# Performance work log

Hardware: AMD Instinct MI355X
Metric: run time of the kernel (lower is better)

Reference implementation:

```python
import jax, jax.numpy as jnp
import numpy as np

B, S, D, H = 2, 2048, 1024, 16
DH = D // H  # dim_per_head = 64


def setup_inputs() -> dict:
    key = jax.random.key(0)
    ks = jax.random.split(key, 12)
    scale = 1.0 / np.sqrt(D)
    inp = {
        "key": jax.random.normal(ks[0], (B, S, D), jnp.float32),
        "value": jax.random.normal(ks[1], (B, S, D), jnp.float32),
        "query": jax.random.normal(ks[2], (B, S, D), jnp.float32),
        "mask": jax.random.randint(ks[3], (B, S, S), 0, 2) == 1,
        "Wq": jax.random.normal(ks[4], (D, D), jnp.float32) * scale,
        "bq": jnp.zeros((D,), jnp.float32),
        "Wk": jax.random.normal(ks[5], (D, D), jnp.float32) * scale,
        "bk": jnp.zeros((D,), jnp.float32),
        "Wv": jax.random.normal(ks[6], (D, D), jnp.float32) * scale,
        "bv": jnp.zeros((D,), jnp.float32),
        "Wo": jax.random.normal(ks[7], (D, D), jnp.float32) * scale,
        "bo": jnp.zeros((D,), jnp.float32),
    }
    return inp


def reference(key, value, query, mask, Wq, bq, Wk, bk, Wv, bv, Wo, bo):
    b, s, d = query.shape
    dh = d // H

    def split_heads(x):  # [b, s, d] -> [b, H, s, dh]
        return x.reshape(b, -1, H, dh).transpose(0, 2, 1, 3)

    q = split_heads(query @ Wq + bq) / jnp.sqrt(jnp.float32(dh))
    k = split_heads(key @ Wk + bk)
    v = split_heads(value @ Wv + bv)

    scores = jnp.einsum("bhqd,bhkd->bhqk", q, k)  # [b, H, s, s]
    scores = jnp.where(mask[:, None, :, :], jnp.float32(-1e18), scores)
    attn = jax.nn.softmax(scores, axis=-1)  # dropout is identity in eval
    ctx = jnp.einsum("bhqk,bhkd->bhqd", attn, v)
    ctx = ctx.transpose(0, 2, 1, 3).reshape(b, s, d)
    return ctx @ Wo + bo
```

## Files before the change

### kernel.cpp

```cpp
#include <hip/hip_runtime.h>
#include <hip/hip_bf16.h>

#define BATCH  2
#define SEQ    2048
#define DMODEL 1024
#define NHEAD  16
#define DHEAD  64
#define NTOK   (BATCH * SEQ)

using f32x4 = __attribute__((ext_vector_type(4))) float;
using s16x4 = __attribute__((ext_vector_type(4))) short;
using s16x8 = __attribute__((ext_vector_type(8))) short;

__device__ __forceinline__ short f2bf(float f) {
  __hip_bfloat16 h = __float2bfloat16(f);
  return *(short*)&h;
}

__device__ __forceinline__ void gload_lds16(const short* g, short* l) {
  __builtin_amdgcn_global_load_lds(
      (const __attribute__((address_space(1))) void*)g,
      (__attribute__((address_space(3))) void*)l, 16, 0, 0);
}

__global__ __launch_bounds__(256) void wtrans_kernel(
    const float* __restrict__ Wq, const float* __restrict__ Wk,
    const float* __restrict__ Wv, const float* __restrict__ Wo,
    short* __restrict__ Wt) {
  __shared__ short tile[64][72];
  const float* W = blockIdx.z == 0 ? Wq : blockIdx.z == 1 ? Wk
                 : blockIdx.z == 2 ? Wv : Wo;
  short* out = Wt + (size_t)blockIdx.z * DMODEL * DMODEL;
  int k0 = blockIdx.x * 64, n0 = blockIdx.y * 64;
  int t = threadIdx.x;
#pragma unroll
  for (int i = 0; i < 4; ++i) {
    int idx = t + i * 256;
    int row = idx >> 4, c4 = idx & 15;
    f32x4 v = *(const f32x4*)(W + (size_t)(k0 + row) * DMODEL + n0 + c4 * 4);
    s16x4 p;
    p[0] = f2bf(v[0]); p[1] = f2bf(v[1]); p[2] = f2bf(v[2]); p[3] = f2bf(v[3]);
    *(s16x4*)&tile[row][c4 * 4] = p;
  }
  __syncthreads();
#pragma unroll
  for (int i = 0; i < 2; ++i) {
    int idx = t + i * 256;
    int nrow = idx >> 3, c8 = idx & 7;
    s16x8 p;
#pragma unroll
    for (int j = 0; j < 8; ++j) p[j] = tile[c8 * 8 + j][nrow];
    *(s16x8*)(out + (size_t)(n0 + nrow) * DMODEL + k0 + c8 * 8) = p;
  }
}

__global__ __launch_bounds__(256) void xcast_kernel(
    const float* __restrict__ Xq, const float* __restrict__ Xk,
    const float* __restrict__ Xv, short* __restrict__ Xb) {
  int sel = blockIdx.y;
  const float* src = sel == 0 ? Xq : sel == 1 ? Xk : Xv;
  size_t off = ((size_t)blockIdx.x * 256 + threadIdx.x) * 8;
  f32x4 v0 = *(const f32x4*)(src + off);
  f32x4 v1 = *(const f32x4*)(src + off + 4);
  s16x8 p;
  p[0] = f2bf(v0[0]); p[1] = f2bf(v0[1]); p[2] = f2bf(v0[2]); p[3] = f2bf(v0[3]);
  p[4] = f2bf(v1[0]); p[5] = f2bf(v1[1]); p[6] = f2bf(v1[2]); p[7] = f2bf(v1[3]);
  *(s16x8*)(Xb + (size_t)sel * NTOK * DMODEL + off) = p;
}

__global__ __launch_bounds__(256) void mpack_kernel(
    const int* __restrict__ mask, unsigned long long* __restrict__ Mp) {
  const int total_words = BATCH * SEQ * (SEQ / 64);
  int lane = threadIdx.x & 63;
  int wv = blockIdx.x * 4 + (threadIdx.x >> 6);
  int nw = gridDim.x * 4;
  for (int w = wv; w < total_words; w += nw) {
    int mv = mask[(size_t)w * 64 + lane];
    unsigned long long bits = __ballot(mv != 0);
    if (lane == 0) Mp[w] = bits;
  }
}

__global__ __launch_bounds__(256) void proj_qkv_kernel(
    const short* __restrict__ Xb, const short* __restrict__ Wt,
    const float* __restrict__ bq, const float* __restrict__ bk,
    const float* __restrict__ bv, short* __restrict__ QKV) {
  __shared__ short As[2][128 * 32];
  __shared__ short Bs[2][128 * 32];
  int wg = blockIdx.x;
  int orig = (wg & 7) * 96 + (wg >> 3);
  int sel = orig >> 8;
  int rem = orig & 255;
  int mx = rem >> 3, ny = rem & 7;

  const short* X    = Xb + (size_t)sel * NTOK * DMODEL;
  const float* bias = sel == 0 ? bq : sel == 1 ? bk : bv;
  const short* Wsel = Wt + (size_t)sel * DMODEL * DMODEL;
  short* Obuf = QKV + (size_t)sel * ((size_t)BATCH * NHEAD * SEQ * DHEAD);
  const float scale = sel == 0 ? 0.18033688011111793f : 1.0f;

  int m0 = mx * 128, n0 = ny * 128;
  int t = threadIdx.x, wid = t >> 6, lane = t & 63;
  int lr = lane & 15, lg = lane >> 4;
  int wr = wid >> 1, wc = wid & 1;
  f32x4 acc[4][4] = {};

  const int gr0 = t >> 2, gc0 = (t & 3) << 3;
  const short* Ax0 = X + (size_t)(m0 + gr0) * DMODEL + gc0;
  const short* Ax1 = Ax0 + (size_t)64 * DMODEL;
  const short* Bw0 = Wsel + (size_t)(n0 + gr0) * DMODEL + gc0;
  const short* Bw1 = Bw0 + (size_t)64 * DMODEL;
  const int lofs0 = (t & ~63) << 3, lofs1 = lofs0 + 256 * 8;

#define STAGEQ(bufi, k0s) {                                                   \
    gload_lds16(Ax0 + (k0s), &As[bufi][0] + lofs0);                           \
    gload_lds16(Ax1 + (k0s), &As[bufi][0] + lofs1);                           \
    gload_lds16(Bw0 + (k0s), &Bs[bufi][0] + lofs0);                           \
    gload_lds16(Bw1 + (k0s), &Bs[bufi][0] + lofs1); }

  STAGEQ(0, 0);
  __syncthreads();

  int cur = 0;
  for (int kt = 0; kt < DMODEL / 32; ++kt) {
    if (kt + 1 < DMODEL / 32) STAGEQ(cur ^ 1, (kt + 1) * 32);
    s16x8 afr[4], bfr[4];
#pragma unroll
    for (int mi = 0; mi < 4; ++mi)
      afr[mi] = *(const s16x8*)(&As[cur][0] + (wr * 64 + mi * 16 + lr) * 32 + lg * 8);
#pragma unroll
    for (int ni = 0; ni < 4; ++ni)
      bfr[ni] = *(const s16x8*)(&Bs[cur][0] + (wc * 64 + ni * 16 + lr) * 32 + lg * 8);
    __builtin_amdgcn_s_setprio(1);
#pragma unroll
    for (int mi = 0; mi < 4; ++mi)
#pragma unroll
      for (int ni = 0; ni < 4; ++ni)
        acc[mi][ni] = __builtin_amdgcn_mfma_f32_16x16x32_bf16(
            afr[mi], bfr[ni], acc[mi][ni], 0, 0, 0);
    __builtin_amdgcn_s_setprio(0);
    __syncthreads();
    cur ^= 1;
  }
#undef STAGEQ

  if (sel == 2) {
    int bq_ = m0 >> 11;
    int s0 = (m0 & (SEQ - 1)) + wr * 64 + lg * 4;
#pragma unroll
    for (int mi = 0; mi < 4; ++mi)
#pragma unroll
      for (int ni = 0; ni < 4; ++ni) {
        int n = n0 + wc * 64 + ni * 16 + lr;
        float bv_ = bias[n];
        int h = n >> 6, d = n & 63;
        s16x4 pk;
#pragma unroll
        for (int r = 0; r < 4; ++r) pk[r] = f2bf(acc[mi][ni][r] + bv_);
        *(s16x4*)&Obuf[((size_t)(bq_ * NHEAD + h) * DHEAD + d) * SEQ
                       + s0 + mi * 16] = pk;
      }
  } else {
#pragma unroll
    for (int mi = 0; mi < 4; ++mi)
#pragma unroll
      for (int ni = 0; ni < 4; ++ni) {
        int n = n0 + wc * 64 + ni * 16 + lr;
        float bv_ = bias[n];
        int h = n >> 6, d = n & 63;
#pragma unroll
        for (int r = 0; r < 4; ++r) {
          int m = m0 + wr * 64 + mi * 16 + lg * 4 + r;
          int b = m >> 11, s = m & (SEQ - 1);
          float val = (acc[mi][ni][r] + bv_) * scale;
          Obuf[((size_t)(b * NHEAD + h) * SEQ + s) * DHEAD + d] = f2bf(val);
        }
      }
  }
}

__global__ __launch_bounds__(256) void attn_kernel(
    const short* __restrict__ Qb, const short* __restrict__ Kb,
    const short* __restrict__ VbT, const unsigned long long* __restrict__ Mp,
    short* __restrict__ Ctx) {
  __shared__ short Ks[2][64 * 64];
  __shared__ short Vt[2][64 * 64];
  __shared__ short Ps[4 * 16 * 64];
  int wg = blockIdx.x;
  int orig = (wg & 7) * 128 + (wg >> 3);
  int bh = orig >> 5, qt = orig & 31;
  int b = bh >> 4, h = bh & 15;
  int q0 = qt * 64;
  int t = threadIdx.x, wid = t >> 6, lane = t & 63;
  int lr = lane & 15, lg = lane >> 4;
  int lr7 = lr & 7;

  const short* Qrow = Qb + ((size_t)bh * SEQ + q0 + wid * 16 + lr) * DHEAD;
  s16x8 qf[2];
  qf[0] = *(const s16x8*)(Qrow + lg * 8);
  qf[1] = *(const s16x8*)(Qrow + 32 + lg * 8);

  const short* KbB = Kb + (size_t)bh * SEQ * DHEAD;
  const short* VtB = VbT + (size_t)bh * DHEAD * SEQ;

  const int srow = lane >> 3;
  const int schunk = ((lane & 7) ^ srow) * 8;

  float m_run = -1e30f, l_run = 0.f;
  f32x4 o_acc[4] = {};

  const unsigned long long* mrow =
      Mp + ((size_t)b * SEQ + q0 + wid * 16 + lr) * (SEQ / 64);

#define STAGE(bufi, k0s)                                                      \
  {                                                                           \
    _Pragma("unroll")                                                         \
    for (int i = 0; i < 2; ++i) {                                             \
      int rbase = wid * 16 + i * 8;                                           \
      gload_lds16(KbB + (size_t)((k0s) + rbase + srow) * DHEAD + schunk,      \
                  &Ks[bufi][rbase * 64]);                                     \
      gload_lds16(VtB + (size_t)(rbase + srow) * SEQ + (k0s) + schunk,        \
                  &Vt[bufi][rbase * 64]);                                     \
    }                                                                         \
  }

  unsigned long long mw_cur = mrow[0];
  STAGE(0, 0);
  asm volatile("s_waitcnt vmcnt(0)" ::: "memory");
  __syncthreads();

  int cur = 0;
  for (int kt = 0; kt < SEQ / 64; ++kt) {
    unsigned long long mw_next = 0;
    if (kt + 1 < SEQ / 64) {
      STAGE(cur ^ 1, (kt + 1) * 64);
      mw_next = mrow[kt + 1];
    }
    const short* KsC = Ks[cur];
    const short* VtC = Vt[cur];

    f32x4 sfr[4];
    __builtin_amdgcn_s_setprio(1);
#pragma unroll
    for (int nf = 0; nf < 4; ++nf) {
      int row = nf * 16 + lr;
      s16x8 kf0 = *(const s16x8*)&KsC[row * 64 + ((lg ^ lr7) << 3)];
      s16x8 kf1 = *(const s16x8*)&KsC[row * 64 + (((4 + lg) ^ lr7) << 3)];
      f32x4 c = {};
      c = __builtin_amdgcn_mfma_f32_16x16x32_bf16(kf0, qf[0], c, 0, 0, 0);
      c = __builtin_amdgcn_mfma_f32_16x16x32_bf16(kf1, qf[1], c, 0, 0, 0);
      sfr[nf] = c;
    }
    __builtin_amdgcn_s_setprio(0);

    unsigned w0 = (unsigned)(mw_cur >> (lg * 4));
    unsigned w1 = (unsigned)(mw_cur >> (lg * 4 + 32));
#pragma unroll
    for (int nf = 0; nf < 4; ++nf)
#pragma unroll
      for (int r = 0; r < 4; ++r) {
        unsigned bit = (nf < 2) ? (w0 >> (nf * 16 + r)) : (w1 >> ((nf - 2) * 16 + r));
        if (bit & 1u) sfr[nf][r] = -1e30f;
      }
    float tm = fmaxf(fmaxf(fmaxf(sfr[0][0], sfr[0][1]), fmaxf(sfr[0][2], sfr[0][3])),
                     fmaxf(fmaxf(sfr[1][0], sfr[1][1]), fmaxf(sfr[1][2], sfr[1][3])));
    float tm2 = fmaxf(fmaxf(fmaxf(sfr[2][0], sfr[2][1]), fmaxf(sfr[2][2], sfr[2][3])),
                      fmaxf(fmaxf(sfr[3][0], sfr[3][1]), fmaxf(sfr[3][2], sfr[3][3])));
    tm = fmaxf(tm, tm2);
    tm = fmaxf(tm, __shfl_xor(tm, 16, 64));
    tm = fmaxf(tm, __shfl_xor(tm, 32, 64));

    bool small = __all(tm <= m_run + 8.0f);
    if (!small) {
      float mnew = fmaxf(m_run, tm);
      float scl = __builtin_amdgcn_exp2f(m_run - mnew);
      m_run = mnew;
      l_run *= scl;
      float scl_o[4];
#pragma unroll
      for (int r = 0; r < 4; ++r) scl_o[r] = __shfl(scl, lg * 4 + r, 64);
#pragma unroll
      for (int nf = 0; nf < 4; ++nf)
#pragma unroll
        for (int r = 0; r < 4; ++r) o_acc[nf][r] *= scl_o[r];
    }
    float ps4[4];
#pragma unroll
    for (int nf = 0; nf < 4; ++nf) {
#pragma unroll
      for (int r = 0; r < 4; ++r)
        sfr[nf][r] = __builtin_amdgcn_exp2f(sfr[nf][r] - m_run);
      ps4[nf] = (sfr[nf][0] + sfr[nf][1]) + (sfr[nf][2] + sfr[nf][3]);
    }
    float ps = (ps4[0] + ps4[1]) + (ps4[2] + ps4[3]);
    ps += __shfl_xor(ps, 16, 64);
    ps += __shfl_xor(ps, 32, 64);
    l_run += ps;

    int psbase = wid * (16 * 64) + lr * 64;
#pragma unroll
    for (int nf = 0; nf < 4; ++nf) {
      s16x4 pk;
#pragma unroll
      for (int r = 0; r < 4; ++r) pk[r] = f2bf(sfr[nf][r]);
      *(s16x4*)&Ps[psbase + ((((2 * nf + (lg >> 1)) ^ lr7) << 3) | ((lg & 1) << 2))] = pk;
    }
    asm volatile("s_waitcnt lgkmcnt(0)" ::: "memory");
    __builtin_amdgcn_sched_barrier(0);

    __builtin_amdgcn_s_setprio(1);
#pragma unroll
    for (int ks = 0; ks < 2; ++ks) {
      s16x8 pf = *(const s16x8*)&Ps[psbase + (((ks * 4 + lg) ^ lr7) << 3)];
#pragma unroll
      for (int nf = 0; nf < 4; ++nf) {
        int d = nf * 16 + lr;
        s16x8 vf = *(const s16x8*)&VtC[d * 64 + (((ks * 4 + lg) ^ lr7) << 3)];
        o_acc[nf] = __builtin_amdgcn_mfma_f32_16x16x32_bf16(pf, vf, o_acc[nf], 0, 0, 0);
      }
    }
    __builtin_amdgcn_s_setprio(0);

    asm volatile("s_waitcnt vmcnt(0)" ::: "memory");
    __syncthreads();
    cur ^= 1;
    mw_cur = mw_next;
  }
#undef STAGE
  float l_o[4];
#pragma unroll
  for (int r = 0; r < 4; ++r) l_o[r] = __shfl(l_run, lg * 4 + r, 64);
#pragma unroll
  for (int nf = 0; nf < 4; ++nf)
#pragma unroll
    for (int r = 0; r < 4; ++r) {
      int srow_ = q0 + wid * 16 + lg * 4 + r;
      float val = o_acc[nf][r] / l_o[r];
      Ctx[((size_t)b * SEQ + srow_) * DMODEL + h * DHEAD + nf * 16 + lr] = f2bf(val);
    }
}

__global__ __launch_bounds__(256) void proj_out_kernel(
    const short* __restrict__ Ctx, const short* __restrict__ Wot,
    const float* __restrict__ bo, float* __restrict__ Out) {
  __shared__ short As[2][128 * 32];
  __shared__ short Bs[2][128 * 32];
  int wg = blockIdx.x;
  int orig = (wg & 7) * 32 + (wg >> 3);
  int mx = orig >> 3, ny = orig & 7;
  int m0 = mx * 128, n0 = ny * 128;
  int t = threadIdx.x, wid = t >> 6, lane = t & 63;
  int lr = lane & 15, lg = lane >> 4;
  int wr = wid >> 1, wc = wid & 1;
  f32x4 acc[4][4] = {};

  const int gr0 = t >> 2, gc0 = (t & 3) << 3;
  const short* Actx0 = Ctx + (size_t)(m0 + gr0) * DMODEL + gc0;
  const short* Actx1 = Actx0 + (size_t)64 * DMODEL;
  const short* Bwo0 = Wot + (size_t)(n0 + gr0) * DMODEL + gc0;
  const short* Bwo1 = Bwo0 + (size_t)64 * DMODEL;
  const int lofs0 = (t & ~63) << 3, lofs1 = lofs0 + 256 * 8;

#define STAGE_PO(bufi, k0s) {                                                 \
    gload_lds16(Actx0 + (k0s), &As[bufi][0] + lofs0);                         \
    gload_lds16(Actx1 + (k0s), &As[bufi][0] + lofs1);                         \
    gload_lds16(Bwo0 + (k0s), &Bs[bufi][0] + lofs0);                          \
    gload_lds16(Bwo1 + (k0s), &Bs[bufi][0] + lofs1); }

  STAGE_PO(0, 0);
  __syncthreads();

  int cur = 0;
  for (int kt = 0; kt < DMODEL / 32; ++kt) {
    if (kt + 1 < DMODEL / 32) STAGE_PO(cur ^ 1, (kt + 1) * 32);
    s16x8 afr[4], bfr[4];
#pragma unroll
    for (int mi = 0; mi < 4; ++mi)
      afr[mi] = *(const s16x8*)(&As[cur][0] + (wr * 64 + mi * 16 + lr) * 32 + lg * 8);
#pragma unroll
    for (int ni = 0; ni < 4; ++ni)
      bfr[ni] = *(const s16x8*)(&Bs[cur][0] + (wc * 64 + ni * 16 + lr) * 32 + lg * 8);
    __builtin_amdgcn_s_setprio(1);
#pragma unroll
    for (int mi = 0; mi < 4; ++mi)
#pragma unroll
      for (int ni = 0; ni < 4; ++ni)
        acc[mi][ni] = __builtin_amdgcn_mfma_f32_16x16x32_bf16(
            afr[mi], bfr[ni], acc[mi][ni], 0, 0, 0);
    __builtin_amdgcn_s_setprio(0);
    __syncthreads();
    cur ^= 1;
  }
#undef STAGE_PO

#pragma unroll
  for (int mi = 0; mi < 4; ++mi)
#pragma unroll
    for (int ni = 0; ni < 4; ++ni) {
      int n = n0 + wc * 64 + ni * 16 + lr;
      float bv_ = bo[n];
#pragma unroll
      for (int r = 0; r < 4; ++r) {
        int m = m0 + wr * 64 + mi * 16 + lg * 4 + r;
        Out[(size_t)m * DMODEL + n] = acc[mi][ni][r] + bv_;
      }
    }
}

extern "C" void kernel_launch(void* const* d_in, const int* in_sizes, int n_in,
                              void* d_out, int out_size, void* d_ws, size_t ws_size,
                              hipStream_t stream) {
  const float* key_in   = (const float*)d_in[0];
  const float* value_in = (const float*)d_in[1];
  const float* query_in = (const float*)d_in[2];
  const int*   mask     = (const int*)d_in[3];
  const float* Wq = (const float*)d_in[4];
  const float* bq = (const float*)d_in[5];
  const float* Wk = (const float*)d_in[6];
  const float* bk = (const float*)d_in[7];
  const float* Wv = (const float*)d_in[8];
  const float* bv = (const float*)d_in[9];
  const float* Wo = (const float*)d_in[10];
  const float* bo = (const float*)d_in[11];
  float* out = (float*)d_out;

  short* ws = (short*)d_ws;
  const size_t WSZ   = (size_t)DMODEL * DMODEL;
  const size_t QKVSZ = (size_t)BATCH * NHEAD * SEQ * DHEAD;
  const size_t XSZ   = (size_t)NTOK * DMODEL;
  short* Wt  = ws;
  short* QKV = ws + 4 * WSZ;
  short* Qb  = QKV;
  short* Kb  = QKV + QKVSZ;
  short* VbT = QKV + 2 * QKVSZ;
  short* Xb  = ws + 4 * WSZ + 3 * QKVSZ;
  short* Ctx = Xb;
  unsigned long long* Mp = (unsigned long long*)ws;

  wtrans_kernel<<<dim3(16, 16, 4), 256, 0, stream>>>(Wq, Wk, Wv, Wo, Wt);
  xcast_kernel<<<dim3(2048, 3), 256, 0, stream>>>(query_in, key_in, value_in, Xb);
  proj_qkv_kernel<<<dim3(768), 256, 0, stream>>>(Xb, Wt, bq, bk, bv, QKV);
  mpack_kernel<<<dim3(1024), 256, 0, stream>>>(mask, Mp);
  attn_kernel<<<dim3(1024), 256, 0, stream>>>(Qb, Kb, VbT, Mp, Ctx);
  proj_out_kernel<<<dim3(256), 256, 0, stream>>>(Ctx, Wt + 3 * WSZ, bo, out);
}
```

Baseline: 189.0 us.

## Use 32x32x16 MFMA in attention with register-resident P and 128-row query tiles

Rewrites the attention kernel so each wave handles 32 query rows with 32x32x16 bf16 MFMAs instead of 16 rows with 16x16x32. The S^T accumulator layout lets P be packed straight from registers into the PV MFMA operand, which removes the LDS round trip and its waitcnt for P. Each workgroup now covers 128 query rows, so the grid is halved and each K/V tile staged in LDS is reused by twice as many queries. The costs are fewer workgroups (512) and larger 16-wide accumulators that raise register pressure, plus more per-element shuffles when rescaling.

New measurement: 183.9 us. -2.7%, faster.

```diff
diff --git a/kernel.cpp b/kernel.cpp
--- a/kernel.cpp
+++ b/kernel.cpp
@@ -8,9 +8,10 @@
 #define DHEAD  64
 #define NTOK   (BATCH * SEQ)
 
-using f32x4 = __attribute__((ext_vector_type(4))) float;
-using s16x4 = __attribute__((ext_vector_type(4))) short;
-using s16x8 = __attribute__((ext_vector_type(8))) short;
+using f32x4  = __attribute__((ext_vector_type(4))) float;
+using f32x16 = __attribute__((ext_vector_type(16))) float;
+using s16x4  = __attribute__((ext_vector_type(4))) short;
+using s16x8  = __attribute__((ext_vector_type(8))) short;
 
 __device__ __forceinline__ short f2bf(float f) {
   __hip_bfloat16 h = __float2bfloat16(f);
@@ -185,20 +186,19 @@
     short* __restrict__ Ctx) {
   __shared__ short Ks[2][64 * 64];
   __shared__ short Vt[2][64 * 64];
-  __shared__ short Ps[4 * 16 * 64];
   int wg = blockIdx.x;
-  int orig = (wg & 7) * 128 + (wg >> 3);
-  int bh = orig >> 5, qt = orig & 31;
+  int orig = (wg & 7) * 64 + (wg >> 3);
+  int bh = orig >> 4, qt = orig & 15;
   int b = bh >> 4, h = bh & 15;
-  int q0 = qt * 64;
+  int q0 = qt * 128;
   int t = threadIdx.x, wid = t >> 6, lane = t & 63;
-  int lr = lane & 15, lg = lane >> 4;
-  int lr7 = lr & 7;
-
-  const short* Qrow = Qb + ((size_t)bh * SEQ + q0 + wid * 16 + lr) * DHEAD;
-  s16x8 qf[2];
-  qf[0] = *(const s16x8*)(Qrow + lg * 8);
-  qf[1] = *(const s16x8*)(Qrow + 32 + lg * 8);
+  int ql = lane & 31, hi = lane >> 5;
+  int qrow = q0 + wid * 32 + ql;
+
+  const short* Qp = Qb + ((size_t)bh * SEQ + qrow) * DHEAD + hi * 8;
+  s16x8 qf[4];
+#pragma unroll
+  for (int ds = 0; ds < 4; ++ds) qf[ds] = *(const s16x8*)(Qp + ds * 16);
 
   const short* KbB = Kb + (size_t)bh * SEQ * DHEAD;
   const short* VtB = VbT + (size_t)bh * DHEAD * SEQ;
@@ -206,11 +206,21 @@
   const int srow = lane >> 3;
   const int schunk = ((lane & 7) ^ srow) * 8;
 
+  int offK[4];
+#pragma unroll
+  for (int j = 0; j < 4; ++j)
+    offK[j] = ql * 64 + (((j * 2 + hi) ^ (ql & 7)) << 3);
+  int offVa[4], offVb[4];
+#pragma unroll
+  for (int m = 0; m < 4; ++m) {
+    offVa[m] = ql * 64 + (((m * 2)     ^ (ql & 7)) << 3) + 4 * hi;
+    offVb[m] = ql * 64 + (((m * 2 + 1) ^ (ql & 7)) << 3) + 4 * hi;
+  }
+
   float m_run = -1e30f, l_run = 0.f;
-  f32x4 o_acc[4] = {};
-
-  const unsigned long long* mrow =
-      Mp + ((size_t)b * SEQ + q0 + wid * 16 + lr) * (SEQ / 64);
+  f32x16 oacc0 = {}, oacc1 = {};
+
+  const unsigned long long* mrow = Mp + ((size_t)b * SEQ + qrow) * (SEQ / 64);
 
 #define STAGE(bufi, k0s)                                                      \
   {                                                                           \
@@ -239,35 +249,31 @@
     const short* KsC = Ks[cur];
     const short* VtC = Vt[cur];
 
-    f32x4 sfr[4];
+    f32x16 sf0 = {}, sf1 = {};
     __builtin_amdgcn_s_setprio(1);
 #pragma unroll
-    for (int nf = 0; nf < 4; ++nf) {
-      int row = nf * 16 + lr;
-      s16x8 kf0 = *(const s16x8*)&KsC[row * 64 + ((lg ^ lr7) << 3)];
-      s16x8 kf1 = *(const s16x8*)&KsC[row * 64 + (((4 + lg) ^ lr7) << 3)];
-      f32x4 c = {};
-      c = __builtin_amdgcn_mfma_f32_16x16x32_bf16(kf0, qf[0], c, 0, 0, 0);
-      c = __builtin_amdgcn_mfma_f32_16x16x32_bf16(kf1, qf[1], c, 0, 0, 0);
-      sfr[nf] = c;
+    for (int ds = 0; ds < 4; ++ds) {
+      s16x8 k0 = *(const s16x8*)&KsC[offK[ds]];
+      s16x8 k1 = *(const s16x8*)&KsC[offK[ds] + 2048];
+      sf0 = __builtin_amdgcn_mfma_f32_32x32x16_bf16(k0, qf[ds], sf0, 0, 0, 0);
+      sf1 = __builtin_amdgcn_mfma_f32_32x32x16_bf16(k1, qf[ds], sf1, 0, 0, 0);
     }
     __builtin_amdgcn_s_setprio(0);
 
-    unsigned w0 = (unsigned)(mw_cur >> (lg * 4));
-    unsigned w1 = (unsigned)(mw_cur >> (lg * 4 + 32));
-#pragma unroll
-    for (int nf = 0; nf < 4; ++nf)
-#pragma unroll
-      for (int r = 0; r < 4; ++r) {
-        unsigned bit = (nf < 2) ? (w0 >> (nf * 16 + r)) : (w1 >> ((nf - 2) * 16 + r));
-        if (bit & 1u) sfr[nf][r] = -1e30f;
-      }
-    float tm = fmaxf(fmaxf(fmaxf(sfr[0][0], sfr[0][1]), fmaxf(sfr[0][2], sfr[0][3])),
-                     fmaxf(fmaxf(sfr[1][0], sfr[1][1]), fmaxf(sfr[1][2], sfr[1][3])));
-    float tm2 = fmaxf(fmaxf(fmaxf(sfr[2][0], sfr[2][1]), fmaxf(sfr[2][2], sfr[2][3])),
-                      fmaxf(fmaxf(sfr[3][0], sfr[3][1]), fmaxf(sfr[3][2], sfr[3][3])));
-    tm = fmaxf(tm, tm2);
-    tm = fmaxf(tm, __shfl_xor(tm, 16, 64));
+    unsigned h0 = ((unsigned)mw_cur) >> (hi << 2);
+    unsigned h1 = ((unsigned)(mw_cur >> 32)) >> (hi << 2);
+#pragma unroll
+    for (int r = 0; r < 16; ++r) {
+      const int c = (r & 3) + 8 * (r >> 2);
+      if ((h0 >> c) & 1u) sf0[r] = -1e30f;
+      if ((h1 >> c) & 1u) sf1[r] = -1e30f;
+    }
+
+    float tm = sf0[0];
+#pragma unroll
+    for (int r = 1; r < 16; ++r) tm = fmaxf(tm, sf0[r]);
+#pragma unroll
+    for (int r = 0; r < 16; ++r) tm = fmaxf(tm, sf1[r]);
     tm = fmaxf(tm, __shfl_xor(tm, 32, 64));
 
     bool small = __all(tm <= m_run + 8.0f);
@@ -276,48 +282,38 @@
       float scl = __builtin_amdgcn_exp2f(m_run - mnew);
       m_run = mnew;
       l_run *= scl;
-      float scl_o[4];
-#pragma unroll
-      for (int r = 0; r < 4; ++r) scl_o[r] = __shfl(scl, lg * 4 + r, 64);
-#pragma unroll
-      for (int nf = 0; nf < 4; ++nf)
-#pragma unroll
-        for (int r = 0; r < 4; ++r) o_acc[nf][r] *= scl_o[r];
-    }
-    float ps4[4];
-#pragma unroll
-    for (int nf = 0; nf < 4; ++nf) {
-#pragma unroll
-      for (int r = 0; r < 4; ++r)
-        sfr[nf][r] = __builtin_amdgcn_exp2f(sfr[nf][r] - m_run);
-      ps4[nf] = (sfr[nf][0] + sfr[nf][1]) + (sfr[nf][2] + sfr[nf][3]);
-    }
-    float ps = (ps4[0] + ps4[1]) + (ps4[2] + ps4[3]);
-    ps += __shfl_xor(ps, 16, 64);
-    ps += __shfl_xor(ps, 32, 64);
-    l_run += ps;
-
-    int psbase = wid * (16 * 64) + lr * 64;
-#pragma unroll
-    for (int nf = 0; nf < 4; ++nf) {
-      s16x4 pk;
-#pragma unroll
-      for (int r = 0; r < 4; ++r) pk[r] = f2bf(sfr[nf][r]);
-      *(s16x4*)&Ps[psbase + ((((2 * nf + (lg >> 1)) ^ lr7) << 3) | ((lg & 1) << 2))] = pk;
-    }
-    asm volatile("s_waitcnt lgkmcnt(0)" ::: "memory");
-    __builtin_amdgcn_sched_barrier(0);
+#pragma unroll
+      for (int r = 0; r < 16; ++r) {
+        float s_ = __shfl(scl, (r & 3) + 8 * (r >> 2) + 4 * hi, 64);
+        oacc0[r] *= s_;
+        oacc1[r] *= s_;
+      }
+    }
+
+    float ss = 0.f;
+#pragma unroll
+    for (int r = 0; r < 16; ++r) {
+      sf0[r] = __builtin_amdgcn_exp2f(sf0[r] - m_run);
+      sf1[r] = __builtin_amdgcn_exp2f(sf1[r] - m_run);
+      ss += sf0[r] + sf1[r];
+    }
+    l_run += ss + __shfl_xor(ss, 32, 64);
 
     __builtin_amdgcn_s_setprio(1);
 #pragma unroll
-    for (int ks = 0; ks < 2; ++ks) {
-      s16x8 pf = *(const s16x8*)&Ps[psbase + (((ks * 4 + lg) ^ lr7) << 3)];
-#pragma unroll
-      for (int nf = 0; nf < 4; ++nf) {
-        int d = nf * 16 + lr;
-        s16x8 vf = *(const s16x8*)&VtC[d * 64 + (((ks * 4 + lg) ^ lr7) << 3)];
-        o_acc[nf] = __builtin_amdgcn_mfma_f32_16x16x32_bf16(pf, vf, o_acc[nf], 0, 0, 0);
-      }
+    for (int m = 0; m < 4; ++m) {
+      const int base = (m & 1) * 8;
+      s16x8 pa;
+#pragma unroll
+      for (int e = 0; e < 8; ++e)
+        pa[e] = f2bf(m < 2 ? sf0[base + e] : sf1[base + e]);
+      union { s16x4 q[2]; s16x8 v; } v0, v1;
+      v0.q[0] = *(const s16x4*)&VtC[offVa[m]];
+      v0.q[1] = *(const s16x4*)&VtC[offVb[m]];
+      v1.q[0] = *(const s16x4*)&VtC[offVa[m] + 2048];
+      v1.q[1] = *(const s16x4*)&VtC[offVb[m] + 2048];
+      oacc0 = __builtin_amdgcn_mfma_f32_32x32x16_bf16(pa, v0.v, oacc0, 0, 0, 0);
+      oacc1 = __builtin_amdgcn_mfma_f32_32x32x16_bf16(pa, v1.v, oacc1, 0, 0, 0);
     }
     __builtin_amdgcn_s_setprio(0);
 
@@ -327,17 +323,16 @@
     mw_cur = mw_next;
   }
 #undef STAGE
-  float l_o[4];
-#pragma unroll
-  for (int r = 0; r < 4; ++r) l_o[r] = __shfl(l_run, lg * 4 + r, 64);
-#pragma unroll
-  for (int nf = 0; nf < 4; ++nf)
-#pragma unroll
-    for (int r = 0; r < 4; ++r) {
-      int srow_ = q0 + wid * 16 + lg * 4 + r;
-      float val = o_acc[nf][r] / l_o[r];
-      Ctx[((size_t)b * SEQ + srow_) * DMODEL + h * DHEAD + nf * 16 + lr] = f2bf(val);
-    }
+
+#pragma unroll
+  for (int r = 0; r < 16; ++r) {
+    int c = (r & 3) + 8 * (r >> 2) + 4 * hi;
+    float linv = 1.0f / __shfl(l_run, c, 64);
+    int q_ = q0 + wid * 32 + c;
+    size_t base = ((size_t)b * SEQ + q_) * DMODEL + h * DHEAD + ql;
+    Ctx[base] = f2bf(oacc0[r] * linv);
+    Ctx[base + 32] = f2bf(oacc1[r] * linv);
+  }
 }
 
 __global__ __launch_bounds__(256) void proj_out_kernel(
@@ -427,7 +422,6 @@
   short* ws = (short*)d_ws;
   const size_t WSZ   = (size_t)DMODEL * DMODEL;
   const size_t QKVSZ = (size_t)BATCH * NHEAD * SEQ * DHEAD;
-  const size_t XSZ   = (size_t)NTOK * DMODEL;
   short* Wt  = ws;
   short* QKV = ws + 4 * WSZ;
   short* Qb  = QKV;
@@ -441,6 +435,6 @@
   xcast_kernel<<<dim3(2048, 3), 256, 0, stream>>>(query_in, key_in, value_in, Xb);
   proj_qkv_kernel<<<dim3(768), 256, 0, stream>>>(Xb, Wt, bq, bk, bv, QKV);
   mpack_kernel<<<dim3(1024), 256, 0, stream>>>(mask, Mp);
-  attn_kernel<<<dim3(1024), 256, 0, stream>>>(Qb, Kb, VbT, Mp, Ctx);
+  attn_kernel<<<dim3(512), 256, 0, stream>>>(Qb, Kb, VbT, Mp, Ctx);
   proj_out_kernel<<<dim3(256), 256, 0, stream>>>(Ctx, Wt + 3 * WSZ, bo, out);
 }
```
